# Kernel optimization log

Hardware: AMD Instinct MI355X
Metric: run time of the kernel (lower is better)

## Reference

```python
import jax, jax.numpy as jnp
import numpy as np
import math

HIDDEN = 1024
HEADS = 16
HEAD_DIM = HIDDEN // HEADS


def setup_inputs() -> dict:
    key = jax.random.key(0)
    ks = jax.random.split(key, 7)
    B, S = 2, 2048
    scale = 1.0 / math.sqrt(HIDDEN)
    return {
        "x": jax.random.normal(ks[0], (B, S, HIDDEN), dtype=jnp.float32),
        "Wq": jax.random.normal(ks[1], (HIDDEN, HIDDEN), dtype=jnp.float32) * scale,
        "Wk": jax.random.normal(ks[2], (HIDDEN, HIDDEN), dtype=jnp.float32) * scale,
        "Wv": jax.random.normal(ks[3], (HIDDEN, HIDDEN), dtype=jnp.float32) * scale,
        "Wo": jax.random.normal(ks[4], (HIDDEN, HIDDEN), dtype=jnp.float32) * scale,
        "quantum_phase": jax.random.normal(ks[5], (HEADS, HEAD_DIM), dtype=jnp.float32),
        "quantum_amplitude": jnp.ones((HEADS, HEAD_DIM), dtype=jnp.float32),
    }


def reference(x, Wq, Wk, Wv, Wo, quantum_phase, quantum_amplitude):
    B, S, d = x.shape
    H, D = HEADS, HEAD_DIM

    # per-head/per-channel quantum modulation: real(x*exp(i*phase)) == x*cos(phase)
    mod = (jnp.cos(quantum_phase) * quantum_amplitude)[None, :, None, :]  # [1,H,1,D]

    def proj(W):
        return (x @ W).reshape(B, S, H, D).transpose(0, 2, 1, 3)  # [B,H,S,D]

    q = proj(Wq) * mod
    k = proj(Wk) * mod
    v = proj(Wv) * mod

    scores = jnp.einsum("bhid,bhjd->bhij", q, k) / math.sqrt(D)  # [B,H,S,S]

    # quantum interference: scores[i,j] *= cos(2*pi*(i-j)/S)
    idx = jnp.arange(S, dtype=jnp.float32)
    cos_mat = jnp.cos(2.0 * math.pi * (idx[:, None] - idx[None, :]) / S)  # [S,S]
    scores = scores * cos_mat

    w = jax.nn.softmax(scores, axis=-1)
    # superposition of attention weights with key-rolled copy
    w = (w + jnp.roll(w, 1, axis=-1)) / math.sqrt(2.0)

    out = jnp.einsum("bhij,bhjd->bhid", w, v)  # [B,H,S,D]
    out = out.transpose(0, 2, 1, 3).reshape(B, S, d)
    return out @ Wo
```

## Files before the change

### kernel.cpp

```cpp
#include <hip/hip_runtime.h>
#include <hip/hip_bf16.h>
#include <math.h>

#define HIDDEN 1024
#define HEADS  16
#define HDIM   64
#define BATCH  2
#define SEQ    2048
#define ROWS   (BATCH*SEQ)
#define BH     (BATCH*HEADS)

typedef __attribute__((ext_vector_type(8))) short  short8;
typedef __attribute__((ext_vector_type(8))) __bf16 bf16x8;
typedef __attribute__((ext_vector_type(4))) float  f32x4;
typedef __attribute__((ext_vector_type(4))) unsigned int uint4v;

static __device__ __forceinline__ unsigned short f2bf(float f) {
    unsigned int u = __builtin_bit_cast(unsigned int, f);
    u += 0x7FFFu + ((u >> 16) & 1u);
    return (unsigned short)(u >> 16);
}
static __device__ __forceinline__ float bf2f(unsigned short h) {
    unsigned int u = ((unsigned int)h) << 16;
    return __builtin_bit_cast(float, u);
}
static __device__ __forceinline__ f32x4 mfma16(short8 a, short8 b, f32x4 c) {
    return __builtin_amdgcn_mfma_f32_16x16x32_bf16(
        __builtin_bit_cast(bf16x8, a), __builtin_bit_cast(bf16x8, b), c, 0, 0, 0);
}
static __device__ __forceinline__ void gl_lds16(const unsigned short* g, unsigned short* l) {
    __builtin_amdgcn_global_load_lds(
        (const __attribute__((address_space(1))) unsigned int*)g,
        (__attribute__((address_space(3))) unsigned int*)l, 16, 0, 0);
}

__global__ __launch_bounds__(256) void prep_kernel(
    const float* __restrict__ x, unsigned short* __restrict__ xb,
    const float* __restrict__ w0, const float* __restrict__ w1,
    const float* __restrict__ w2, const float* __restrict__ w3,
    unsigned short* __restrict__ wt,
    const float* __restrict__ qp, const float* __restrict__ qa,
    float* __restrict__ mod, float* __restrict__ mod2,
    float* __restrict__ posc, float* __restrict__ poss) {
    __shared__ unsigned short tile[64][72];
    const int bid = blockIdx.x;
    const int t = threadIdx.x;
    if (bid < 4096) {
        int i = (bid * 256 + t) * 4;
        float4 v = *(const float4*)(x + i);
        ushort4 o;
        o.x = f2bf(v.x); o.y = f2bf(v.y); o.z = f2bf(v.z); o.w = f2bf(v.w);
        *(ushort4*)(xb + i) = o;
        if (bid < 8) {
            int k = bid * 256 + t;
            if (k < HIDDEN) {
                float m = cosf(qp[k]) * qa[k];
                mod[k] = m;
                mod2[k] = m * m * 0.18033688011112042f;
            }
            if (k < SEQ) {
                float ang = (float)k * (6.283185307179586f / (float)SEQ);
                posc[k] = cosf(ang);
                poss[k] = sinf(ang);
            }
        }
        return;
    }
    int rem = bid - 4096;
    int z = rem >> 8, r2 = rem & 255;
    int n0 = (r2 & 15) * 64, k0 = (r2 >> 4) * 64;
    const float* src = (z == 0) ? w0 : (z == 1) ? w1 : (z == 2) ? w2 : w3;
    unsigned short* dst = wt + (size_t)z * HIDDEN * HIDDEN;
    int cg = t & 15, r0 = t >> 4;
#pragma unroll
    for (int rr = 0; rr < 4; rr++) {
        int kl = r0 + rr * 16;
        float4 v = *(const float4*)(src + (size_t)(k0 + kl) * HIDDEN + n0 + cg * 4);
        tile[cg*4+0][kl] = f2bf(v.x);
        tile[cg*4+1][kl] = f2bf(v.y);
        tile[cg*4+2][kl] = f2bf(v.z);
        tile[cg*4+3][kl] = f2bf(v.w);
    }
    __syncthreads();
#pragma unroll
    for (int rr = 0; rr < 4; rr++) {
        int nl = r0 + rr * 16;
        ushort4 o;
        o.x = tile[nl][cg*4+0]; o.y = tile[nl][cg*4+1];
        o.z = tile[nl][cg*4+2]; o.w = tile[nl][cg*4+3];
        *(ushort4*)(dst + (size_t)(n0 + nl) * HIDDEN + k0 + cg * 4) = o;
    }
}

__global__ __launch_bounds__(256) void gemm_kernel(
    const unsigned short* __restrict__ A, const unsigned short* __restrict__ WtBase,
    unsigned short* __restrict__ CBase, const float* __restrict__ mod) {
    __shared__ unsigned short Alds[128 * 64];
    __shared__ unsigned short Blds[64 * 64];
    const int mode = blockIdx.z;
    const unsigned short* Bt = WtBase + (size_t)mode * HIDDEN * HIDDEN;
    unsigned short* Cout = CBase + (size_t)mode * ROWS * HIDDEN;
    const int m0 = blockIdx.x * 128, n0 = blockIdx.y * 64;
    const int tid = threadIdx.x;
    const int wave = tid >> 6, lane = tid & 63, quad = lane >> 4, l15 = lane & 15;
    const int wr = wave >> 1, wc = wave & 1;
    const int srow = lane >> 3;
    const int schunk = (lane & 7) ^ (srow & 7);

    f32x4 acc[4][2];
    const f32x4 z4 = {0.f, 0.f, 0.f, 0.f};
#pragma unroll
    for (int i = 0; i < 4; i++)
#pragma unroll
        for (int j = 0; j < 2; j++) acc[i][j] = z4;

    for (int k0 = 0; k0 < HIDDEN; k0 += 64) {
#pragma unroll
        for (int p = 0; p < 4; p++) {
            int rbase = p * 32 + wave * 8;
            gl_lds16(A + (size_t)(m0 + rbase + srow) * HIDDEN + k0 + schunk * 8,
                     &Alds[rbase * 64]);
        }
#pragma unroll
        for (int p = 0; p < 2; p++) {
            int rbase = p * 32 + wave * 8;
            gl_lds16(Bt + (size_t)(n0 + rbase + srow) * HIDDEN + k0 + schunk * 8,
                     &Blds[rbase * 64]);
        }
        __syncthreads();
        short8 aF[4][2], bF[2][2];
#pragma unroll
        for (int h = 0; h < 2; h++) {
#pragma unroll
            for (int i = 0; i < 4; i++) {
                int row = wr * 64 + i * 16 + l15;
                aF[i][h] = *(const short8*)(&Alds[row * 64 + ((h * 4 + quad) ^ (l15 & 7)) * 8]);
            }
#pragma unroll
            for (int j = 0; j < 2; j++) {
                int row = wc * 32 + j * 16 + l15;
                bF[j][h] = *(const short8*)(&Blds[row * 64 + ((h * 4 + quad) ^ (l15 & 7)) * 8]);
            }
        }
#pragma unroll
        for (int h = 0; h < 2; h++)
#pragma unroll
            for (int i = 0; i < 4; i++)
#pragma unroll
                for (int j = 0; j < 2; j++)
                    acc[i][j] = mfma16(aF[i][h], bF[j][h], acc[i][j]);
        __syncthreads();
    }

#pragma unroll
    for (int i = 0; i < 4; i++) {
        int mbase = m0 + wr * 64 + i * 16 + quad * 4;
#pragma unroll
        for (int j = 0; j < 2; j++) {
            int n = n0 + wc * 32 + j * 16 + l15;
            float vm = (mode == 2) ? mod[n] : 1.0f;
#pragma unroll
            for (int r = 0; r < 4; r++) {
                int mm = mbase + r;
                Cout[(size_t)mm * HIDDEN + n] = f2bf(acc[i][j][r] * vm);
            }
        }
    }
}

__global__ __launch_bounds__(256) void gemm_o_kernel(
    const unsigned short* __restrict__ A, const unsigned short* __restrict__ Bt,
    float* __restrict__ Out) {
    __shared__ unsigned short Alds[128 * 64];
    __shared__ unsigned short Blds[64 * 64];
    const int m0 = blockIdx.x * 128, n0 = blockIdx.y * 64;
    const int tid = threadIdx.x;
    const int wave = tid >> 6, lane = tid & 63, quad = lane >> 4, l15 = lane & 15;
    const int wr = wave >> 1, wc = wave & 1;
    const int srow = lane >> 3;
    const int schunk = (lane & 7) ^ (srow & 7);

    f32x4 acc[4][2];
    const f32x4 z4 = {0.f, 0.f, 0.f, 0.f};
#pragma unroll
    for (int i = 0; i < 4; i++)
#pragma unroll
        for (int j = 0; j < 2; j++) acc[i][j] = z4;

    for (int k0 = 0; k0 < HIDDEN; k0 += 64) {
#pragma unroll
        for (int p = 0; p < 4; p++) {
            int rbase = p * 32 + wave * 8;
            gl_lds16(A + (size_t)(m0 + rbase + srow) * HIDDEN + k0 + schunk * 8,
                     &Alds[rbase * 64]);
        }
#pragma unroll
        for (int p = 0; p < 2; p++) {
            int rbase = p * 32 + wave * 8;
            gl_lds16(Bt + (size_t)(n0 + rbase + srow) * HIDDEN + k0 + schunk * 8,
                     &Blds[rbase * 64]);
        }
        __syncthreads();
        short8 aF[4][2], bF[2][2];
#pragma unroll
        for (int h = 0; h < 2; h++) {
#pragma unroll
            for (int i = 0; i < 4; i++) {
                int row = wr * 64 + i * 16 + l15;
                aF[i][h] = *(const short8*)(&Alds[row * 64 + ((h * 4 + quad) ^ (l15 & 7)) * 8]);
            }
#pragma unroll
            for (int j = 0; j < 2; j++) {
                int row = wc * 32 + j * 16 + l15;
                bF[j][h] = *(const short8*)(&Blds[row * 64 + ((h * 4 + quad) ^ (l15 & 7)) * 8]);
            }
        }
#pragma unroll
        for (int h = 0; h < 2; h++)
#pragma unroll
            for (int i = 0; i < 4; i++)
#pragma unroll
                for (int j = 0; j < 2; j++)
                    acc[i][j] = mfma16(aF[i][h], bF[j][h], acc[i][j]);
        __syncthreads();
    }

#pragma unroll
    for (int i = 0; i < 4; i++) {
        int mbase = m0 + wr * 64 + i * 16 + quad * 4;
#pragma unroll
        for (int j = 0; j < 2; j++) {
            int n = n0 + wc * 32 + j * 16 + l15;
#pragma unroll
            for (int r = 0; r < 4; r++)
                Out[(size_t)(mbase + r) * HIDDEN + n] = acc[i][j][r];
        }
    }
}

__global__ __launch_bounds__(256) void vshift_kernel(const unsigned short* __restrict__ Vm,
                                                     unsigned short* __restrict__ Vpt) {
    __shared__ unsigned short lds[65][72];
    int bh = blockIdx.x, b = bh >> 4, h = bh & 15;
    int s0 = blockIdx.y * 64;
    int t = threadIdx.x;
    int cg = t & 15, r0 = t >> 4;
#pragma unroll
    for (int rr = 0; rr < 4; rr++) {
        int row = r0 + rr * 16;
        ushort4 v = *(const ushort4*)(Vm + ((size_t)(b * SEQ + s0 + row)) * HIDDEN + h * 64 + cg * 4);
        *(ushort4*)(&lds[row][cg * 4]) = v;
    }
    if (t < 16) {
        int srow = (s0 + 64) & (SEQ - 1);
        ushort4 v = *(const ushort4*)(Vm + ((size_t)(b * SEQ + srow)) * HIDDEN + h * 64 + t * 4);
        *(ushort4*)(&lds[64][t * 4]) = v;
    }
    __syncthreads();
    int d = t & 63, sb = (t >> 6) * 16;
    unsigned short outv[16];
#pragma unroll
    for (int k = 0; k < 16; k++) {
        float a = bf2f(lds[sb + k][d]), bb = bf2f(lds[sb + k + 1][d]);
        outv[k] = f2bf((a + bb) * 0.7071067811865476f);
    }
    unsigned short* dst = Vpt + ((size_t)bh * 64 + d) * SEQ + s0 + sb;
#pragma unroll
    for (int k = 0; k < 16; k += 4) {
        ushort4 o; o.x = outv[k]; o.y = outv[k+1]; o.z = outv[k+2]; o.w = outv[k+3];
        *(ushort4*)(dst + k) = o;
    }
}

#define KT 128
__global__ __launch_bounds__(256) void attn_kernel(const unsigned short* __restrict__ Cq,
                                                   const unsigned short* __restrict__ Ck,
                                                   const unsigned short* __restrict__ Vpt,
                                                   unsigned short* __restrict__ Ob,
                                                   const float* __restrict__ mod2,
                                                   const float* __restrict__ posc,
                                                   const float* __restrict__ poss) {
    __shared__ unsigned short Klds[2][KT * 64];
    __shared__ unsigned short Vtlds[2][64 * 128];
    const int bh = blockIdx.x;
    const int b = bh >> 4, h = bh & 15;
    const int tid = threadIdx.x, wave = tid >> 6, lane = tid & 63;
    const int quad = lane >> 4, l15 = lane & 15;
    const int q0 = blockIdx.y * 128 + wave * 32;

    short8 qf[2][2];
#pragma unroll
    for (int g = 0; g < 2; g++) {
        int ss = q0 + g * 16 + l15;
        const unsigned short* crow = Cq + ((size_t)(b * SEQ + ss)) * HIDDEN + h * 64;
#pragma unroll
        for (int kk = 0; kk < 2; kk++) {
            int bd = kk * 32 + quad * 8;
            short8 u = *(const short8*)(crow + bd);
            short8 q;
#pragma unroll
            for (int e = 0; e < 8; e++)
                q[e] = (short)f2bf(bf2f((unsigned short)u[e]) * mod2[h * 64 + bd + e]);
            qf[g][kk] = q;
        }
    }
    float ci_[2], si_[2];
#pragma unroll
    for (int g = 0; g < 2; g++) {
        ci_[g] = posc[q0 + g * 16 + l15];
        si_[g] = poss[q0 + g * 16 + l15];
    }

    short8 ones;
#pragma unroll
    for (int e = 0; e < 8; e++) ones[e] = (short)0x3F80;

    const f32x4 z4 = {0.f, 0.f, 0.f, 0.f};
    f32x4 acc[2][4], accden[2];
#pragma unroll
    for (int g = 0; g < 2; g++) {
#pragma unroll
        for (int dt = 0; dt < 4; dt++) acc[g][dt] = z4;
        accden[g] = z4;
    }

    const unsigned short* Kbh = Ck  + ((size_t)b * SEQ) * HIDDEN + h * 64;
    const unsigned short* Vbh = Vpt + (size_t)bh * 64 * SEQ;

    auto stage = [&](int j, int buf) {
#pragma unroll
        for (int p = 0; p < 4; p++) {
            int rb = p * 32 + wave * 8;
            int r  = rb + (lane >> 3);
            int c  = (lane & 7) ^ (r & 7);
            gl_lds16(Kbh + (size_t)(j + r) * HIDDEN + c * 8, &Klds[buf][rb * 64]);
        }
#pragma unroll
        for (int p = 0; p < 4; p++) {
            int rb = p * 16 + wave * 4;
            int r  = rb + (lane >> 4);
            int c  = (lane & 15) ^ (r & 15);
            gl_lds16(Vbh + (size_t)r * SEQ + j + c * 8, &Vtlds[buf][rb * 128]);
        }
    };

    stage(0, 0);
    const int NIT = SEQ / KT;
    for (int it = 0; it < NIT; it++) {
        __syncthreads();
        if (it + 1 < NIT) stage((it + 1) * KT, (it + 1) & 1);
        const int buf = it & 1;

#pragma unroll
        for (int chunk = 0; chunk < 4; chunk++) {
            const int jb = it * KT + chunk * 32 + quad * 4;
            f32x4 cjA[2], sjA[2];
            cjA[0] = *(const f32x4*)(posc + jb);
            sjA[0] = *(const f32x4*)(poss + jb);
            cjA[1] = *(const f32x4*)(posc + jb + 16);
            sjA[1] = *(const f32x4*)(poss + jb + 16);

            f32x4 sc[2][2];
            sc[0][0] = z4; sc[0][1] = z4; sc[1][0] = z4; sc[1][1] = z4;
            __builtin_amdgcn_s_setprio(1);
#pragma unroll
            for (int t2i = 0; t2i < 2; t2i++) {
                int tt = chunk * 2 + t2i;
#pragma unroll
                for (int kk = 0; kk < 2; kk++) {
                    int ch = (kk * 4 + quad) ^ (l15 & 7);
                    short8 kf = *(const short8*)(&Klds[buf][(tt * 16 + l15) * 64 + ch * 8]);
                    sc[0][t2i] = mfma16(kf, qf[0][kk], sc[0][t2i]);
                    sc[1][t2i] = mfma16(kf, qf[1][kk], sc[1][t2i]);
                }
            }
            __builtin_amdgcn_s_setprio(0);

            short8 pa[2];
#pragma unroll
            for (int g = 0; g < 2; g++) {
                unsigned int w_[4];
#pragma unroll
                for (int t2i = 0; t2i < 2; t2i++) {
#pragma unroll
                    for (int hp = 0; hp < 2; hp++) {
                        float wl = ci_[g] * cjA[t2i][2 * hp]     + si_[g] * sjA[t2i][2 * hp];
                        float wh = ci_[g] * cjA[t2i][2 * hp + 1] + si_[g] * sjA[t2i][2 * hp + 1];
                        float pl = __builtin_amdgcn_exp2f(sc[g][t2i][2 * hp]     * wl);
                        float ph = __builtin_amdgcn_exp2f(sc[g][t2i][2 * hp + 1] * wh);
                        unsigned int w;
                        asm("v_cvt_pk_bf16_f32 %0, %1, %2" : "=v"(w) : "v"(pl), "v"(ph));
                        w_[t2i * 2 + hp] = w;
                    }
                }
                auto t02 = __builtin_amdgcn_permlane32_swap(w_[0], w_[2], false, false);
                auto a02 = __builtin_amdgcn_permlane16_swap(t02[0], t02[1], false, false);
                auto t13 = __builtin_amdgcn_permlane32_swap(w_[1], w_[3], false, false);
                auto a13 = __builtin_amdgcn_permlane16_swap(t13[0], t13[1], false, false);
                uint4v pword;
                pword[0] = a02[0]; pword[1] = a13[0]; pword[2] = a02[1]; pword[3] = a13[1];
                pa[g] = __builtin_bit_cast(short8, pword);
                accden[g] = mfma16(pa[g], ones, accden[g]);
            }

            __builtin_amdgcn_s_setprio(1);
#pragma unroll
            for (int dt = 0; dt < 4; dt++) {
                int ch = (chunk * 4 + quad) ^ l15;
                short8 vb = *(const short8*)(&Vtlds[buf][(dt * 16 + l15) * 128 + ch * 8]);
                acc[0][dt] = mfma16(pa[0], vb, acc[0][dt]);
                acc[1][dt] = mfma16(pa[1], vb, acc[1][dt]);
            }
            __builtin_amdgcn_s_setprio(0);
        }
    }

#pragma unroll
    for (int g = 0; g < 2; g++) {
        float rinv[4];
#pragma unroll
        for (int r = 0; r < 4; r++) rinv[r] = 1.0f / accden[g][r];
#pragma unroll
        for (int dt = 0; dt < 4; dt++) {
#pragma unroll
            for (int r = 0; r < 4; r++) {
                int q = q0 + g * 16 + quad * 4 + r;
                int d = dt * 16 + l15;
                Ob[((size_t)(b * SEQ + q)) * HIDDEN + h * 64 + d] = f2bf(acc[g][dt][r] * rinv[r]);
            }
        }
    }
}

extern "C" void kernel_launch(void* const* d_in, const int* in_sizes, int n_in,
                              void* d_out, int out_size, void* d_ws, size_t ws_size,
                              hipStream_t stream) {
    const float* x  = (const float*)d_in[0];
    const float* Wq = (const float*)d_in[1];
    const float* Wk = (const float*)d_in[2];
    const float* Wv = (const float*)d_in[3];
    const float* Wo = (const float*)d_in[4];
    const float* qp = (const float*)d_in[5];
    const float* qa = (const float*)d_in[6];
    char* ws = (char*)d_ws;

    unsigned short* Xb  = (unsigned short*)(ws);
    unsigned short* Wt  = (unsigned short*)(ws + (size_t)( 8 << 20));
    unsigned short* Cq  = (unsigned short*)(ws + (size_t)(16 << 20));
    unsigned short* Ck  = (unsigned short*)(ws + (size_t)(24 << 20));
    unsigned short* Cv  = (unsigned short*)(ws + (size_t)(32 << 20));
    unsigned short* Vpt = (unsigned short*)(ws + (size_t)(40 << 20));
    float* mod  = (float*)(ws + (size_t)(48 << 20));
    float* mod2 = mod + 1024;
    float* posc = mod2 + 1024;
    float* poss = posc + 2048;
    float* out  = (float*)d_out;

    prep_kernel<<<5120, 256, 0, stream>>>(x, Xb, Wq, Wk, Wv, Wo, Wt,
                                          qp, qa, mod, mod2, posc, poss);
    gemm_kernel<<<dim3(32, 16, 3), 256, 0, stream>>>(Xb, Wt, Cq, mod);
    vshift_kernel<<<dim3(32, 32), 256, 0, stream>>>(Cv, Vpt);
    attn_kernel<<<dim3(32, 16), 256, 0, stream>>>(Cq, Ck, Vpt, Xb , mod2, posc, poss);
    gemm_o_kernel<<<dim3(32, 16), 256, 0, stream>>>(Xb, Wt + (size_t)3 * HIDDEN * HIDDEN, out);
}
```

Baseline: 216.9 us.

## Use 8 waves per attention block with 16 query rows each, single-buffered LDS

The attention kernel now launches 512 threads per block, each wave handling 16 query rows instead of 32. K/V tiles are single-buffered with a sync before and after compute, replacing the previous double-buffered prefetch. This halves per-wave registers and LDS to raise occupancy, but gives up explicit load/compute overlap within a block and halves K-fragment reuse across query groups.

Result: no change. 212.9 us (-1.8%).

```diff
diff --git a/kernel.cpp b/kernel.cpp
--- a/kernel.cpp
+++ b/kernel.cpp
@@ -273,26 +273,24 @@
 }
 
 #define KT 128
-__global__ __launch_bounds__(256) void attn_kernel(const unsigned short* __restrict__ Cq,
-                                                   const unsigned short* __restrict__ Ck,
-                                                   const unsigned short* __restrict__ Vpt,
-                                                   unsigned short* __restrict__ Ob,
-                                                   const float* __restrict__ mod2,
-                                                   const float* __restrict__ posc,
-                                                   const float* __restrict__ poss) {
-    __shared__ unsigned short Klds[2][KT * 64];
-    __shared__ unsigned short Vtlds[2][64 * 128];
+__global__ __launch_bounds__(512, 4) void attn_kernel(const unsigned short* __restrict__ Cq,
+                                                      const unsigned short* __restrict__ Ck,
+                                                      const unsigned short* __restrict__ Vpt,
+                                                      unsigned short* __restrict__ Ob,
+                                                      const float* __restrict__ mod2,
+                                                      const float* __restrict__ posc,
+                                                      const float* __restrict__ poss) {
+    __shared__ unsigned short Klds[KT * 64];
+    __shared__ unsigned short Vtlds[64 * 128];
     const int bh = blockIdx.x;
     const int b = bh >> 4, h = bh & 15;
     const int tid = threadIdx.x, wave = tid >> 6, lane = tid & 63;
     const int quad = lane >> 4, l15 = lane & 15;
-    const int q0 = blockIdx.y * 128 + wave * 32;
-
-    short8 qf[2][2];
-#pragma unroll
-    for (int g = 0; g < 2; g++) {
-        int ss = q0 + g * 16 + l15;
-        const unsigned short* crow = Cq + ((size_t)(b * SEQ + ss)) * HIDDEN + h * 64;
+    const int q0 = blockIdx.y * 128 + wave * 16;
+
+    short8 qf[2];
+    {
+        const unsigned short* crow = Cq + ((size_t)(b * SEQ + q0 + l15)) * HIDDEN + h * 64;
 #pragma unroll
         for (int kk = 0; kk < 2; kk++) {
             int bd = kk * 32 + quad * 8;
@@ -301,55 +299,46 @@
 #pragma unroll
             for (int e = 0; e < 8; e++)
                 q[e] = (short)f2bf(bf2f((unsigned short)u[e]) * mod2[h * 64 + bd + e]);
-            qf[g][kk] = q;
-        }
-    }
-    float ci_[2], si_[2];
-#pragma unroll
-    for (int g = 0; g < 2; g++) {
-        ci_[g] = posc[q0 + g * 16 + l15];
-        si_[g] = poss[q0 + g * 16 + l15];
-    }
+            qf[kk] = q;
+        }
+    }
+    const float ci_ = posc[q0 + l15];
+    const float si_ = poss[q0 + l15];
 
     short8 ones;
 #pragma unroll
     for (int e = 0; e < 8; e++) ones[e] = (short)0x3F80;
 
     const f32x4 z4 = {0.f, 0.f, 0.f, 0.f};
-    f32x4 acc[2][4], accden[2];
-#pragma unroll
-    for (int g = 0; g < 2; g++) {
-#pragma unroll
-        for (int dt = 0; dt < 4; dt++) acc[g][dt] = z4;
-        accden[g] = z4;
-    }
+    f32x4 acc[4], accden;
+#pragma unroll
+    for (int dt = 0; dt < 4; dt++) acc[dt] = z4;
+    accden = z4;
 
     const unsigned short* Kbh = Ck  + ((size_t)b * SEQ) * HIDDEN + h * 64;
     const unsigned short* Vbh = Vpt + (size_t)bh * 64 * SEQ;
 
-    auto stage = [&](int j, int buf) {
-#pragma unroll
-        for (int p = 0; p < 4; p++) {
-            int rb = p * 32 + wave * 8;
+    auto stage = [&](int j) {
+#pragma unroll
+        for (int p = 0; p < 2; p++) {
+            int rb = p * 64 + wave * 8;
             int r  = rb + (lane >> 3);
             int c  = (lane & 7) ^ (r & 7);
-            gl_lds16(Kbh + (size_t)(j + r) * HIDDEN + c * 8, &Klds[buf][rb * 64]);
-        }
-#pragma unroll
-        for (int p = 0; p < 4; p++) {
-            int rb = p * 16 + wave * 4;
+            gl_lds16(Kbh + (size_t)(j + r) * HIDDEN + c * 8, &Klds[rb * 64]);
+        }
+#pragma unroll
+        for (int p = 0; p < 2; p++) {
+            int rb = p * 32 + wave * 4;
             int r  = rb + (lane >> 4);
             int c  = (lane & 15) ^ (r & 15);
-            gl_lds16(Vbh + (size_t)r * SEQ + j + c * 8, &Vtlds[buf][rb * 128]);
+            gl_lds16(Vbh + (size_t)r * SEQ + j + c * 8, &Vtlds[rb * 128]);
         }
     };
 
-    stage(0, 0);
     const int NIT = SEQ / KT;
     for (int it = 0; it < NIT; it++) {
-        __syncthreads();
-        if (it + 1 < NIT) stage((it + 1) * KT, (it + 1) & 1);
-        const int buf = it & 1;
+        stage(it * KT);
+        __syncthreads();
 
 #pragma unroll
         for (int chunk = 0; chunk < 4; chunk++) {
@@ -360,8 +349,8 @@
             cjA[1] = *(const f32x4*)(posc + jb + 16);
             sjA[1] = *(const f32x4*)(poss + jb + 16);
 
-            f32x4 sc[2][2];
-            sc[0][0] = z4; sc[0][1] = z4; sc[1][0] = z4; sc[1][1] = z4;
+            f32x4 sc[2];
+            sc[0] = z4; sc[1] = z4;
             __builtin_amdgcn_s_setprio(1);
 #pragma unroll
             for (int t2i = 0; t2i < 2; t2i++) {
@@ -369,65 +358,60 @@
 #pragma unroll
                 for (int kk = 0; kk < 2; kk++) {
                     int ch = (kk * 4 + quad) ^ (l15 & 7);
-                    short8 kf = *(const short8*)(&Klds[buf][(tt * 16 + l15) * 64 + ch * 8]);
-                    sc[0][t2i] = mfma16(kf, qf[0][kk], sc[0][t2i]);
-                    sc[1][t2i] = mfma16(kf, qf[1][kk], sc[1][t2i]);
+                    short8 kf = *(const short8*)(&Klds[(tt * 16 + l15) * 64 + ch * 8]);
+                    sc[t2i] = mfma16(kf, qf[kk], sc[t2i]);
                 }
             }
             __builtin_amdgcn_s_setprio(0);
 
-            short8 pa[2];
-#pragma unroll
-            for (int g = 0; g < 2; g++) {
-                unsigned int w_[4];
-#pragma unroll
-                for (int t2i = 0; t2i < 2; t2i++) {
-#pragma unroll
-                    for (int hp = 0; hp < 2; hp++) {
-                        float wl = ci_[g] * cjA[t2i][2 * hp]     + si_[g] * sjA[t2i][2 * hp];
-                        float wh = ci_[g] * cjA[t2i][2 * hp + 1] + si_[g] * sjA[t2i][2 * hp + 1];
-                        float pl = __builtin_amdgcn_exp2f(sc[g][t2i][2 * hp]     * wl);
-                        float ph = __builtin_amdgcn_exp2f(sc[g][t2i][2 * hp + 1] * wh);
-                        unsigned int w;
-                        asm("v_cvt_pk_bf16_f32 %0, %1, %2" : "=v"(w) : "v"(pl), "v"(ph));
-                        w_[t2i * 2 + hp] = w;
-                    }
+            unsigned int w_[4];
+#pragma unroll
+            for (int t2i = 0; t2i < 2; t2i++) {
+#pragma unroll
+                for (int hp = 0; hp < 2; hp++) {
+                    float wl = ci_ * cjA[t2i][2 * hp]     + si_ * sjA[t2i][2 * hp];
+                    float wh = ci_ * cjA[t2i][2 * hp + 1] + si_ * sjA[t2i][2 * hp + 1];
+                    float pl = __builtin_amdgcn_exp2f(sc[t2i][2 * hp]     * wl);
+                    float ph = __builtin_amdgcn_exp2f(sc[t2i][2 * hp + 1] * wh);
+                    unsigned int w;
+                    asm("v_cvt_pk_bf16_f32 %0, %1, %2" : "=v"(w) : "v"(pl), "v"(ph));
+                    w_[t2i * 2 + hp] = w;
                 }
+            }
+            short8 pa;
+            {
                 auto t02 = __builtin_amdgcn_permlane32_swap(w_[0], w_[2], false, false);
                 auto a02 = __builtin_amdgcn_permlane16_swap(t02[0], t02[1], false, false);
                 auto t13 = __builtin_amdgcn_permlane32_swap(w_[1], w_[3], false, false);
                 auto a13 = __builtin_amdgcn_permlane16_swap(t13[0], t13[1], false, false);
                 uint4v pword;
                 pword[0] = a02[0]; pword[1] = a13[0]; pword[2] = a02[1]; pword[3] = a13[1];
-                pa[g] = __builtin_bit_cast(short8, pword);
-                accden[g] = mfma16(pa[g], ones, accden[g]);
-            }
+                pa = __builtin_bit_cast(short8, pword);
+            }
+            accden = mfma16(pa, ones, accden);
 
             __builtin_amdgcn_s_setprio(1);
 #pragma unroll
             for (int dt = 0; dt < 4; dt++) {
                 int ch = (chunk * 4 + quad) ^ l15;
-                short8 vb = *(const short8*)(&Vtlds[buf][(dt * 16 + l15) * 128 + ch * 8]);
-                acc[0][dt] = mfma16(pa[0], vb, acc[0][dt]);
-                acc[1][dt] = mfma16(pa[1], vb, acc[1][dt]);
+                short8 vb = *(const short8*)(&Vtlds[(dt * 16 + l15) * 128 + ch * 8]);
+                acc[dt] = mfma16(pa, vb, acc[dt]);
             }
             __builtin_amdgcn_s_setprio(0);
         }
-    }
-
-#pragma unroll
-    for (int g = 0; g < 2; g++) {
-        float rinv[4];
-#pragma unroll
-        for (int r = 0; r < 4; r++) rinv[r] = 1.0f / accden[g][r];
-#pragma unroll
-        for (int dt = 0; dt < 4; dt++) {
-#pragma unroll
-            for (int r = 0; r < 4; r++) {
-                int q = q0 + g * 16 + quad * 4 + r;
-                int d = dt * 16 + l15;
-                Ob[((size_t)(b * SEQ + q)) * HIDDEN + h * 64 + d] = f2bf(acc[g][dt][r] * rinv[r]);
-            }
+        __syncthreads();
+    }
+
+    float rinv[4];
+#pragma unroll
+    for (int r = 0; r < 4; r++) rinv[r] = 1.0f / accden[r];
+#pragma unroll
+    for (int dt = 0; dt < 4; dt++) {
+#pragma unroll
+        for (int r = 0; r < 4; r++) {
+            int q = q0 + quad * 4 + r;
+            int d = dt * 16 + l15;
+            Ob[((size_t)(b * SEQ + q)) * HIDDEN + h * 64 + d] = f2bf(acc[dt][r] * rinv[r]);
         }
     }
 }
@@ -460,6 +444,6 @@
                                           qp, qa, mod, mod2, posc, poss);
     gemm_kernel<<<dim3(32, 16, 3), 256, 0, stream>>>(Xb, Wt, Cq, mod);
     vshift_kernel<<<dim3(32, 32), 256, 0, stream>>>(Cv, Vpt);
-    attn_kernel<<<dim3(32, 16), 256, 0, stream>>>(Cq, Ck, Vpt, Xb , mod2, posc, poss);
+    attn_kernel<<<dim3(32, 16), 512, 0, stream>>>(Cq, Ck, Vpt, Xb , mod2, posc, poss);
     gemm_o_kernel<<<dim3(32, 16), 256, 0, stream>>>(Xb, Wt + (size_t)3 * HIDDEN * HIDDEN, out);
 }
```

## Split attention keys across two wave groups and fuse QKV GEMMs per block

Applied to the files above, without the earlier changes.

The QKV projection kernel now computes all three outputs in one block, reusing the A tile from LDS across the Q, K and V weights instead of launching a z-dimension of three. The attention kernel doubles to 512 threads. Two groups of four waves each process half of the key sequence, and their partial numerators and denominators are combined through LDS at the end. The aim is more parallelism and latency hiding per query tile and less redundant A loading. In exchange, the cross-iteration double-buffer prefetch is dropped (loads are now issued and synchronized each iteration), and the QKV kernel launches fewer blocks with more accumulator registers.

After: 206.3 us. 1.05x faster.

```diff
diff --git a/kernel.cpp b/kernel.cpp
--- a/kernel.cpp
+++ b/kernel.cpp
@@ -96,10 +96,7 @@
     const unsigned short* __restrict__ A, const unsigned short* __restrict__ WtBase,
     unsigned short* __restrict__ CBase, const float* __restrict__ mod) {
     __shared__ unsigned short Alds[128 * 64];
-    __shared__ unsigned short Blds[64 * 64];
-    const int mode = blockIdx.z;
-    const unsigned short* Bt = WtBase + (size_t)mode * HIDDEN * HIDDEN;
-    unsigned short* Cout = CBase + (size_t)mode * ROWS * HIDDEN;
+    __shared__ unsigned short Blds[3][64 * 64];
     const int m0 = blockIdx.x * 128, n0 = blockIdx.y * 64;
     const int tid = threadIdx.x;
     const int wave = tid >> 6, lane = tid & 63, quad = lane >> 4, l15 = lane & 15;
@@ -107,12 +104,14 @@
     const int srow = lane >> 3;
     const int schunk = (lane & 7) ^ (srow & 7);
 
-    f32x4 acc[4][2];
+    f32x4 acc[3][4][2];
     const f32x4 z4 = {0.f, 0.f, 0.f, 0.f};
 #pragma unroll
-    for (int i = 0; i < 4; i++)
-#pragma unroll
-        for (int j = 0; j < 2; j++) acc[i][j] = z4;
+    for (int z = 0; z < 3; z++)
+#pragma unroll
+        for (int i = 0; i < 4; i++)
+#pragma unroll
+            for (int j = 0; j < 2; j++) acc[z][i][j] = z4;
 
     for (int k0 = 0; k0 < HIDDEN; k0 += 64) {
 #pragma unroll
@@ -122,47 +121,60 @@
                      &Alds[rbase * 64]);
         }
 #pragma unroll
-        for (int p = 0; p < 2; p++) {
-            int rbase = p * 32 + wave * 8;
-            gl_lds16(Bt + (size_t)(n0 + rbase + srow) * HIDDEN + k0 + schunk * 8,
-                     &Blds[rbase * 64]);
+        for (int z = 0; z < 3; z++) {
+#pragma unroll
+            for (int p = 0; p < 2; p++) {
+                int rbase = p * 32 + wave * 8;
+                gl_lds16(WtBase + (size_t)z * HIDDEN * HIDDEN
+                             + (size_t)(n0 + rbase + srow) * HIDDEN + k0 + schunk * 8,
+                         &Blds[z][rbase * 64]);
+            }
         }
         __syncthreads();
-        short8 aF[4][2], bF[2][2];
-#pragma unroll
-        for (int h = 0; h < 2; h++) {
+        short8 aF[4][2];
+#pragma unroll
+        for (int h = 0; h < 2; h++)
 #pragma unroll
             for (int i = 0; i < 4; i++) {
                 int row = wr * 64 + i * 16 + l15;
                 aF[i][h] = *(const short8*)(&Alds[row * 64 + ((h * 4 + quad) ^ (l15 & 7)) * 8]);
             }
 #pragma unroll
+        for (int z = 0; z < 3; z++) {
+            short8 bF[2][2];
+#pragma unroll
+            for (int h = 0; h < 2; h++)
+#pragma unroll
+                for (int j = 0; j < 2; j++) {
+                    int row = wc * 32 + j * 16 + l15;
+                    bF[j][h] = *(const short8*)(&Blds[z][row * 64 + ((h * 4 + quad) ^ (l15 & 7)) * 8]);
+                }
+#pragma unroll
+            for (int h = 0; h < 2; h++)
+#pragma unroll
+                for (int i = 0; i < 4; i++)
+#pragma unroll
+                    for (int j = 0; j < 2; j++)
+                        acc[z][i][j] = mfma16(aF[i][h], bF[j][h], acc[z][i][j]);
+        }
+        __syncthreads();
+    }
+
+#pragma unroll
+    for (int z = 0; z < 3; z++) {
+        unsigned short* Cout = CBase + (size_t)z * ROWS * HIDDEN;
+#pragma unroll
+        for (int i = 0; i < 4; i++) {
+            int mbase = m0 + wr * 64 + i * 16 + quad * 4;
+#pragma unroll
             for (int j = 0; j < 2; j++) {
-                int row = wc * 32 + j * 16 + l15;
-                bF[j][h] = *(const short8*)(&Blds[row * 64 + ((h * 4 + quad) ^ (l15 & 7)) * 8]);
-            }
-        }
-#pragma unroll
-        for (int h = 0; h < 2; h++)
-#pragma unroll
-            for (int i = 0; i < 4; i++)
-#pragma unroll
-                for (int j = 0; j < 2; j++)
-                    acc[i][j] = mfma16(aF[i][h], bF[j][h], acc[i][j]);
-        __syncthreads();
-    }
-
-#pragma unroll
-    for (int i = 0; i < 4; i++) {
-        int mbase = m0 + wr * 64 + i * 16 + quad * 4;
-#pragma unroll
-        for (int j = 0; j < 2; j++) {
-            int n = n0 + wc * 32 + j * 16 + l15;
-            float vm = (mode == 2) ? mod[n] : 1.0f;
-#pragma unroll
-            for (int r = 0; r < 4; r++) {
-                int mm = mbase + r;
-                Cout[(size_t)mm * HIDDEN + n] = f2bf(acc[i][j][r] * vm);
+                int n = n0 + wc * 32 + j * 16 + l15;
+                float vm = (z == 2) ? mod[n] : 1.0f;
+#pragma unroll
+                for (int r = 0; r < 4; r++) {
+                    int mm = mbase + r;
+                    Cout[(size_t)mm * HIDDEN + n] = f2bf(acc[z][i][j][r] * vm);
+                }
             }
         }
     }
@@ -273,20 +285,22 @@
 }
 
 #define KT 128
-__global__ __launch_bounds__(256) void attn_kernel(const unsigned short* __restrict__ Cq,
-                                                   const unsigned short* __restrict__ Ck,
-                                                   const unsigned short* __restrict__ Vpt,
-                                                   unsigned short* __restrict__ Ob,
-                                                   const float* __restrict__ mod2,
-                                                   const float* __restrict__ posc,
-                                                   const float* __restrict__ poss) {
-    __shared__ unsigned short Klds[2][KT * 64];
-    __shared__ unsigned short Vtlds[2][64 * 128];
+__global__ __launch_bounds__(512, 4) void attn_kernel(const unsigned short* __restrict__ Cq,
+                                                      const unsigned short* __restrict__ Ck,
+                                                      const unsigned short* __restrict__ Vpt,
+                                                      unsigned short* __restrict__ Ob,
+                                                      const float* __restrict__ mod2,
+                                                      const float* __restrict__ posc,
+                                                      const float* __restrict__ poss) {
+    __shared__ unsigned short sbuf[2 * KT * 64 + 2 * 64 * KT];
+    unsigned short* KldsB  = sbuf;
+    unsigned short* VtldsB = sbuf + 2 * KT * 64;
     const int bh = blockIdx.x;
     const int b = bh >> 4, h = bh & 15;
     const int tid = threadIdx.x, wave = tid >> 6, lane = tid & 63;
+    const int kh = wave >> 2, w4 = wave & 3;
     const int quad = lane >> 4, l15 = lane & 15;
-    const int q0 = blockIdx.y * 128 + wave * 32;
+    const int q0 = blockIdx.y * 128 + w4 * 32;
 
     short8 qf[2][2];
 #pragma unroll
@@ -327,33 +341,40 @@
     const unsigned short* Kbh = Ck  + ((size_t)b * SEQ) * HIDDEN + h * 64;
     const unsigned short* Vbh = Vpt + (size_t)bh * 64 * SEQ;
 
-    auto stage = [&](int j, int buf) {
-#pragma unroll
-        for (int p = 0; p < 4; p++) {
-            int rb = p * 32 + wave * 8;
-            int r  = rb + (lane >> 3);
-            int c  = (lane & 7) ^ (r & 7);
-            gl_lds16(Kbh + (size_t)(j + r) * HIDDEN + c * 8, &Klds[buf][rb * 64]);
-        }
-#pragma unroll
-        for (int p = 0; p < 4; p++) {
-            int rb = p * 16 + wave * 4;
-            int r  = rb + (lane >> 4);
-            int c  = (lane & 15) ^ (r & 15);
-            gl_lds16(Vbh + (size_t)r * SEQ + j + c * 8, &Vtlds[buf][rb * 128]);
+    auto stage = [&](int it) {
+#pragma unroll
+        for (int t = 0; t < 2; t++) {
+            const int j = t * (SEQ / 2) + it * KT;
+            unsigned short* Kd = KldsB  + t * KT * 64;
+            unsigned short* Vd = VtldsB + t * 64 * KT;
+#pragma unroll
+            for (int p = 0; p < 2; p++) {
+                int rb = p * 64 + wave * 8;
+                int r  = rb + (lane >> 3);
+                int c  = (lane & 7) ^ (r & 7);
+                gl_lds16(Kbh + (size_t)(j + r) * HIDDEN + c * 8, Kd + rb * 64);
+            }
+#pragma unroll
+            for (int p = 0; p < 2; p++) {
+                int rb = p * 32 + wave * 4;
+                int r  = rb + (lane >> 4);
+                int c  = (lane & 15) ^ (r & 15);
+                gl_lds16(Vbh + (size_t)r * SEQ + j + c * 8, Vd + rb * KT);
+            }
         }
     };
 
-    stage(0, 0);
-    const int NIT = SEQ / KT;
+    const unsigned short* Kme = KldsB  + kh * KT * 64;
+    const unsigned short* Vme = VtldsB + kh * 64 * KT;
+    const int NIT = (SEQ / 2) / KT;
     for (int it = 0; it < NIT; it++) {
+        stage(it);
         __syncthreads();
-        if (it + 1 < NIT) stage((it + 1) * KT, (it + 1) & 1);
-        const int buf = it & 1;
+        const int jbase = kh * (SEQ / 2) + it * KT;
 
 #pragma unroll
         for (int chunk = 0; chunk < 4; chunk++) {
-            const int jb = it * KT + chunk * 32 + quad * 4;
+            const int jb = jbase + chunk * 32 + quad * 4;
             f32x4 cjA[2], sjA[2];
             cjA[0] = *(const f32x4*)(posc + jb);
             sjA[0] = *(const f32x4*)(poss + jb);
@@ -369,7 +390,7 @@
 #pragma unroll
                 for (int kk = 0; kk < 2; kk++) {
                     int ch = (kk * 4 + quad) ^ (l15 & 7);
-                    short8 kf = *(const short8*)(&Klds[buf][(tt * 16 + l15) * 64 + ch * 8]);
+                    short8 kf = *(const short8*)(Kme + (tt * 16 + l15) * 64 + ch * 8);
                     sc[0][t2i] = mfma16(kf, qf[0][kk], sc[0][t2i]);
                     sc[1][t2i] = mfma16(kf, qf[1][kk], sc[1][t2i]);
                 }
@@ -407,26 +428,56 @@
 #pragma unroll
             for (int dt = 0; dt < 4; dt++) {
                 int ch = (chunk * 4 + quad) ^ l15;
-                short8 vb = *(const short8*)(&Vtlds[buf][(dt * 16 + l15) * 128 + ch * 8]);
+                short8 vb = *(const short8*)(Vme + (dt * 16 + l15) * KT + ch * 8);
                 acc[0][dt] = mfma16(pa[0], vb, acc[0][dt]);
                 acc[1][dt] = mfma16(pa[1], vb, acc[1][dt]);
             }
             __builtin_amdgcn_s_setprio(0);
         }
-    }
-
-#pragma unroll
-    for (int g = 0; g < 2; g++) {
-        float rinv[4];
-#pragma unroll
-        for (int r = 0; r < 4; r++) rinv[r] = 1.0f / accden[g][r];
-#pragma unroll
-        for (int dt = 0; dt < 4; dt++) {
-#pragma unroll
-            for (int r = 0; r < 4; r++) {
-                int q = q0 + g * 16 + quad * 4 + r;
-                int d = dt * 16 + l15;
-                Ob[((size_t)(b * SEQ + q)) * HIDDEN + h * 64 + d] = f2bf(acc[g][dt][r] * rinv[r]);
+        __syncthreads();
+    }
+
+    float* cmb = (float*)sbuf;
+    const int slot = (w4 * 64 + lane) * 41;
+    if (kh == 1) {
+#pragma unroll
+        for (int g = 0; g < 2; g++) {
+#pragma unroll
+            for (int dt = 0; dt < 4; dt++)
+#pragma unroll
+                for (int r = 0; r < 4; r++)
+                    cmb[slot + g * 16 + dt * 4 + r] = acc[g][dt][r];
+#pragma unroll
+            for (int r = 0; r < 4; r++)
+                cmb[slot + 32 + g * 4 + r] = accden[g][r];
+        }
+    }
+    __syncthreads();
+    if (kh == 0) {
+#pragma unroll
+        for (int g = 0; g < 2; g++) {
+#pragma unroll
+            for (int dt = 0; dt < 4; dt++)
+#pragma unroll
+                for (int r = 0; r < 4; r++)
+                    acc[g][dt][r] += cmb[slot + g * 16 + dt * 4 + r];
+#pragma unroll
+            for (int r = 0; r < 4; r++)
+                accden[g][r] += cmb[slot + 32 + g * 4 + r];
+        }
+#pragma unroll
+        for (int g = 0; g < 2; g++) {
+            float rinv[4];
+#pragma unroll
+            for (int r = 0; r < 4; r++) rinv[r] = 1.0f / accden[g][r];
+#pragma unroll
+            for (int dt = 0; dt < 4; dt++) {
+#pragma unroll
+                for (int r = 0; r < 4; r++) {
+                    int q = q0 + g * 16 + quad * 4 + r;
+                    int d = dt * 16 + l15;
+                    Ob[((size_t)(b * SEQ + q)) * HIDDEN + h * 64 + d] = f2bf(acc[g][dt][r] * rinv[r]);
+                }
             }
         }
     }
@@ -458,8 +509,8 @@
 
     prep_kernel<<<5120, 256, 0, stream>>>(x, Xb, Wq, Wk, Wv, Wo, Wt,
                                           qp, qa, mod, mod2, posc, poss);
-    gemm_kernel<<<dim3(32, 16, 3), 256, 0, stream>>>(Xb, Wt, Cq, mod);
+    gemm_kernel<<<dim3(32, 16), 256, 0, stream>>>(Xb, Wt, Cq, mod);
     vshift_kernel<<<dim3(32, 32), 256, 0, stream>>>(Cv, Vpt);
-    attn_kernel<<<dim3(32, 16), 256, 0, stream>>>(Cq, Ck, Vpt, Xb , mod2, posc, poss);
+    attn_kernel<<<dim3(32, 16), 512, 0, stream>>>(Cq, Ck, Vpt, Xb , mod2, posc, poss);
     gemm_o_kernel<<<dim3(32, 16), 256, 0, stream>>>(Xb, Wt + (size_t)3 * HIDDEN * HIDDEN, out);
 }
```
